# Kernel tuning notes

Hardware: AMD Instinct MI355X
Metric: run time of the kernel (lower is better)

The kernel has to match this reference:

```python
import jax, jax.numpy as jnp
import numpy as np
from jax import lax

K, N, DV, NBPS, NITER, BATCH = 1056, 2112, 5, 4, 20, 1024
M = N - K            # number of parity checks
E = M * (DV + 1)     # Tanner-graph edges (H = [A | I_m], row weight DV+1)
NSYM = N // NBPS     # QAM symbols per codeword


def _qam16():
    # Sionna-style Gray-mapped QAM constellation, unit average energy.
    def pam_gray(b):
        if len(b) > 1:
            return (1 - 2 * b[0]) * (2 ** (len(b) - 1) - pam_gray(b[1:]))
        return 1 - 2 * b[0]
    pts = []
    for i in range(2 ** NBPS):
        b = [(i >> (NBPS - 1 - j)) & 1 for j in range(NBPS)]
        pts.append(complex(pam_gray(b[0::2]), pam_gray(b[1::2])))
    pts = np.asarray(pts)
    pts = pts / np.sqrt(np.mean(np.abs(pts) ** 2))
    return pts.real.astype(np.float32), pts.imag.astype(np.float32)


def setup_inputs() -> dict:
    key = jax.random.key(0)
    rng = np.random.default_rng(0)
    bits = jnp.asarray(rng.integers(0, 2, size=(BATCH, K)), jnp.int32)
    # sparse A: DV distinct info-bit columns per check row
    a_idx = np.argsort(rng.random((M, K)), axis=1)[:, :DV].astype(np.int32)
    edge_vn = np.concatenate([a_idx, K + np.arange(M, dtype=np.int32)[:, None]], axis=1).reshape(-1)
    edge_cn = np.repeat(np.arange(M, dtype=np.int32), DV + 1)
    pre, pim = _qam16()
    k1, k2 = jax.random.split(key)
    return {
        "bits": bits,
        "a_idx": jnp.asarray(a_idx),
        "edge_cn": jnp.asarray(edge_cn),
        "edge_vn": jnp.asarray(edge_vn),
        "points_re": jnp.asarray(pre),
        "points_im": jnp.asarray(pim),
        "noise_re": jax.random.normal(k1, (BATCH, NSYM), jnp.float32),
        "noise_im": jax.random.normal(k2, (BATCH, NSYM), jnp.float32),
        "ebno_db": jnp.float32(4.0),
    }


def _forward(bits, a_idx, edge_cn, edge_vn, points_re, points_im, noise_re, noise_im, ebno_db):
    B = bits.shape[0]
    coderate = K / N
    # ebnodb2no (Es = 1): N0 = 1 / (EbN0_lin * coderate * bits_per_symbol)
    no = 1.0 / (10.0 ** (ebno_db / 10.0) * coderate * NBPS)
    # --- LDPC encode: H = [A | I], parity_i = XOR of info bits in row i ---
    parity = jnp.sum(bits[:, a_idx], axis=-1) % 2          # [B, M]
    cw = jnp.concatenate([bits, parity], axis=1)           # [B, N]
    # --- QAM map ---
    w = jnp.array([1 << (NBPS - 1 - j) for j in range(NBPS)], jnp.int32)
    sym = jnp.sum(cw.reshape(B, NSYM, NBPS) * w, axis=-1)  # [B, S]
    sigma = jnp.sqrt(no / 2.0)
    y_re = points_re[sym] + sigma * noise_re
    y_im = points_im[sym] + sigma * noise_im
    # --- APP demap: LLR = log p(b=0|y) - log p(b=1|y) ---
    d2 = (y_re[..., None] - points_re) ** 2 + (y_im[..., None] - points_im) ** 2  # [B,S,16]
    lg = (-d2 / no)[..., None]                                                     # [B,S,16,1]
    lab = (jnp.arange(2 ** NBPS)[:, None] >> jnp.arange(NBPS - 1, -1, -1)) & 1     # [16,4]
    NEG = jnp.float32(-1e30)
    l0 = jax.nn.logsumexp(jnp.where(lab == 0, lg, NEG), axis=2)
    l1 = jax.nn.logsumexp(jnp.where(lab == 1, lg, NEG), axis=2)
    llr = (l0 - l1).reshape(B, N)                          # [B, N]
    # --- sum-product BP, flooding schedule, NITER iterations ---
    def marg(c2v):  # scatter-add check->variable messages onto variable nodes
        return jnp.zeros((B, N), c2v.dtype).at[:, edge_vn].add(c2v)
    def step(c2v, _):
        v2c = (llr + marg(c2v))[:, edge_vn] - c2v          # extrinsic VN->CN [B,E]
        av = jnp.clip(jnp.abs(v2c), 1e-6, 20.0)
        lt = jnp.log(jnp.tanh(av * 0.5))                   # log|tanh(.)| <= 0
        sg = (v2c < 0).astype(v2c.dtype)
        cs = jnp.zeros((B, M), v2c.dtype).at[:, edge_cn].add(lt)
        ns = jnp.zeros((B, M), v2c.dtype).at[:, edge_cn].add(sg)
        ex = jnp.exp(jnp.minimum(cs[:, edge_cn] - lt, -1e-7))   # prod over other edges < 1
        sp = 1.0 - 2.0 * jnp.mod(ns[:, edge_cn] - sg, 2.0)      # sign product over other edges
        return sp * 2.0 * jnp.arctanh(ex), None
    c2v, _ = lax.scan(step, jnp.zeros((B, E), jnp.float32), None, length=NITER)
    tot = llr + marg(c2v)
    bits_rx = (tot[:, :K] < 0).astype(jnp.float32)         # hard_out=True
    return bits.astype(jnp.float32), bits_rx, tot[:, :K]


def reference(bits, a_idx, edge_cn, edge_vn, points_re, points_im, noise_re, noise_im, ebno_db):
    b, brx, _ = _forward(bits, a_idx, edge_cn, edge_vn, points_re, points_im,
                         noise_re, noise_im, ebno_db)
    return b, brx
```

## Files before the change

### kernel.cpp

```cpp
#include <hip/hip_runtime.h>

#define K_     1056
#define N_     2112
#define M_     1056
#define E_     6336
#define NIE_   5280
#define CAP_   6336
#define ALL_   7392
#define DV_    5
#define ROW_   6
#define NSYM_  528
#define NITER_ 20
#define BATCH_ 1024
#define BS_    512

#define LOG2E_ 1.4426950408889634f
#define AVLO_  (1e-6f * LOG2E_)
#define AVHI_  (20.0f * LOG2E_)
#define QC_    0.99999988f

__device__ __forceinline__ int seg_stride(int d) { return d | 1; }

__device__ __forceinline__ float fexp2(float x) { return __builtin_amdgcn_exp2f(x); }
__device__ __forceinline__ float flog2(float x) { return __builtin_amdgcn_logf(x); }
__device__ __forceinline__ float frcp(float x)  { return __builtin_amdgcn_rcpf(x); }

__global__ __launch_bounds__(BS_, 8) void link_kernel(
    const int*   __restrict__ bits,
    const int*   __restrict__ a_idx,
    const float* __restrict__ points_re,
    const float* __restrict__ points_im,
    const float* __restrict__ noise_re,
    const float* __restrict__ noise_im,
    const float* __restrict__ ebno_db,
    const int*   __restrict__ edge_vn,
    float*       __restrict__ out)
{
#pragma clang fp contract(off)
    const int b   = blockIdx.x;
    const int tid = threadIdx.x;

    __shared__ float s_all[ALL_];
    __shared__ float s_pre[16];
    __shared__ float s_pim[16];
    __shared__ int   s_hist[32];
    __shared__ int   s_binStart[32];
    __shared__ int   s_binBase[32];

    float* s_mem  = s_all;
    float* s_marg = s_all + CAP_;

    int* sc        = (int*)(s_all + N_);
    int* s_deg     = sc;
    int* s_perm    = sc + K_;
    int* s_offslot = sc + 2 * K_;
    int* s_cnt     = sc + 3 * K_;

    if (tid < 16) {
        s_pre[tid] = points_re[tid];
        s_pim[tid] = points_im[tid];
    }
    if (tid < 32) s_hist[tid] = 0;

    const float eb    = ebno_db[0];
    const float no    = 1.0f / ((powf(10.0f, eb / 10.0f) * 0.5f) * 4.0f);
    const float sigma = sqrtf(no / 2.0f);

    for (int i = tid; i < K_; i += BS_) {
        int v = bits[b * K_ + i];
        s_mem[i] = (float)v;
        out[b * K_ + i] = (float)v;
    }
    __syncthreads();

    for (int m = tid; m < M_; m += BS_) {
        float acc = 0.0f;
        #pragma unroll
        for (int d = 0; d < DV_; ++d) acc += s_mem[a_idx[m * DV_ + d]];
        s_mem[K_ + m] = (float)(((int)acc) & 1);
    }
    for (int v = tid; v < K_; v += BS_) { s_deg[v] = 0; s_cnt[v] = 0; }
    __syncthreads();

    for (int s = tid; s < NSYM_; s += BS_) {
        int c0 = (int)s_mem[4 * s + 0];
        int c1 = (int)s_mem[4 * s + 1];
        int c2 = (int)s_mem[4 * s + 2];
        int c3 = (int)s_mem[4 * s + 3];
        int sym = c0 * 8 + c1 * 4 + c2 * 2 + c3;
        float yre = s_pre[sym] + sigma * noise_re[b * NSYM_ + s];
        float yim = s_pim[sym] + sigma * noise_im[b * NSYM_ + s];
        #pragma unroll
        for (int j = 0; j < 4; ++j) {
            float m0 = -1e30f, m1 = -1e30f;
            #pragma unroll
            for (int p = 0; p < 16; ++p) {
                float dre  = yre - s_pre[p];
                float dim_ = yim - s_pim[p];
                float lg   = -(dre * dre + dim_ * dim_) / no;
                if (((p >> (3 - j)) & 1) == 0) m0 = fmaxf(m0, lg);
                else                           m1 = fmaxf(m1, lg);
            }
            float sum0 = 0.0f, sum1 = 0.0f;
            #pragma unroll
            for (int p = 0; p < 16; ++p) {
                float dre  = yre - s_pre[p];
                float dim_ = yim - s_pim[p];
                float lg   = -(dre * dre + dim_ * dim_) / no;
                if (((p >> (3 - j)) & 1) == 0) sum0 += __expf(lg - m0);
                else                           sum1 += __expf(lg - m1);
            }
            float llr = (m0 + __logf(sum0)) - (m1 + __logf(sum1));
            s_mem[4 * s + j] = llr * LOG2E_;
        }
    }
    for (int idx = tid; idx < NIE_; idx += BS_) {
        int m = idx / 5, j = idx - m * 5;
        atomicAdd(&s_deg[edge_vn[m * ROW_ + j]], 1);
    }
    __syncthreads();

    for (int v = tid; v < K_; v += BS_) atomicAdd(&s_hist[s_deg[v] & 31], 1);
    __syncthreads();
    if (tid == 0) {
        int accS = 0, accB = 0;
        for (int d = 0; d < 32; ++d) {
            int c = s_hist[d];
            s_binStart[d] = accS;
            s_binBase[d]  = accB;
            s_hist[d]     = accS;
            accS += c;
            accB += c * seg_stride(d);
        }
    }
    __syncthreads();
    for (int v = tid; v < K_; v += BS_) {
        int d    = s_deg[v];
        int slot = atomicAdd(&s_hist[d & 31], 1);
        int base = s_binBase[d] + (slot - s_binStart[d]) * seg_stride(d);
        s_perm[slot]  = v | (d << 16);
        s_offslot[v]  = base | (slot << 16);
    }
    __syncthreads();

    int      pv[3];
    unsigned od[3];
    float    lr[3];
    #pragma unroll
    for (int k = 0; k < 3; ++k) {
        int s = tid + BS_ * k;
        if (s < K_) {
            int w = s_perm[s];
            int v = w & 0xFFFF;
            int d = w >> 16;
            int base = s_binBase[d] + (s - s_binStart[d]) * seg_stride(d);
            pv[k] = v;
            od[k] = (unsigned)base | ((unsigned)d << 16);
            lr[k] = s_mem[v];
        } else { pv[k] = 0; od[k] = 0; lr[k] = 0.0f; }
    }
    float    t5[3];
    unsigned vnp[3][5];
    #pragma unroll
    for (int kk = 0; kk < 3; ++kk) {
        int m = tid + BS_ * kk;
        if (m < M_) {
            #pragma unroll
            for (int j = 0; j < 5; ++j) {
                int v = edge_vn[m * ROW_ + j];
                int r = atomicAdd(&s_cnt[v], 1);
                int w = s_offslot[v];
                vnp[kk][j]  = (unsigned)(w >> 16) | ((unsigned)((w & 0xFFFF) + r) << 16);
            }
            float lrP = s_mem[K_ + m];
            float av  = __builtin_amdgcn_fmed3f(fabsf(lrP), AVLO_, AVHI_);
            float e   = fexp2(-av);
            float tm  = (1.0f - e) * frcp(1.0f + e);
            t5[kk] = copysignf(tm, lrP);
        } else { t5[kk] = 0.0f; }
    }
    __syncthreads();
    for (int i = tid; i < CAP_; i += BS_) s_mem[i] = 0.0f;
    __syncthreads();

    for (int it = 0; it < NITER_; ++it) {
        #pragma unroll
        for (int k = 0; k < 3; ++k) {
            int s = tid + BS_ * k;
            if (s < K_) {
                int base = (int)(od[k] & 0xFFFFu);
                int dg   = (int)(od[k] >> 16);
                float mg = lr[k];
                int d = 0;
                for (; d + 1 < dg; d += 2) {
                    mg += s_mem[base + d];
                    mg += s_mem[base + d + 1];
                }
                if (d < dg) mg += s_mem[base + d];
                s_marg[s] = mg;
            }
        }
        __syncthreads();
        #pragma unroll
        for (int kk = 0; kk < 3; ++kk) {
            int m = tid + BS_ * kk;
            if (m < M_) {
                float tj[5];
                #pragma unroll
                for (int j = 0; j < 5; ++j) {
                    unsigned w = vnp[kk][j];
                    float v2c = s_marg[w & 0xFFFFu] - s_mem[w >> 16];
                    float av  = __builtin_amdgcn_fmed3f(fabsf(v2c), AVLO_, AVHI_);
                    float e   = fexp2(-av);
                    float tm  = (1.0f - e) * frcp(1.0f + e);
                    tj[j] = copysignf(tm, v2c);
                }
                float qv[5];
                float pr = t5[kk];
                #pragma unroll
                for (int j = 0; j < 5; ++j) { qv[j] = pr; pr *= tj[j]; }
                float sf = 1.0f;
                #pragma unroll
                for (int j = 4; j >= 0; --j) { qv[j] *= sf; sf *= tj[j]; }
                #pragma unroll
                for (int j = 0; j < 5; ++j) {
                    float q = __builtin_amdgcn_fmed3f(qv[j], -QC_, QC_);
                    float r = flog2((1.0f + q) * frcp(1.0f - q));
                    s_mem[vnp[kk][j] >> 16] = r;
                }
            }
        }
        __syncthreads();
    }

    #pragma unroll
    for (int k = 0; k < 3; ++k) {
        int s = tid + BS_ * k;
        if (s < K_) {
            int base = (int)(od[k] & 0xFFFFu);
            int dg   = (int)(od[k] >> 16);
            float mg = lr[k];
            int d = 0;
            for (; d + 1 < dg; d += 2) {
                mg += s_mem[base + d];
                mg += s_mem[base + d + 1];
            }
            if (d < dg) mg += s_mem[base + d];
            out[(size_t)BATCH_ * K_ + b * K_ + pv[k]] = (mg < 0.0f) ? 1.0f : 0.0f;
        }
    }
}

extern "C" void kernel_launch(void* const* d_in, const int* in_sizes, int n_in,
                              void* d_out, int out_size, void* d_ws, size_t ws_size,
                              hipStream_t stream) {
    const int*   bits    = (const int*)  d_in[0];
    const int*   a_idx   = (const int*)  d_in[1];
    const int*   edge_vn = (const int*)  d_in[3];
    const float* pre     = (const float*)d_in[4];
    const float* pim     = (const float*)d_in[5];
    const float* nre     = (const float*)d_in[6];
    const float* nim     = (const float*)d_in[7];
    const float* ebno    = (const float*)d_in[8];

    link_kernel<<<BATCH_, BS_, 0, stream>>>(bits, a_idx, pre, pim, nre, nim,
                                            ebno, edge_vn, (float*)d_out);
}
```

Before: 183.9 us.

## Write extrinsic VN messages in place and pack edge byte offsets

The variable-node pass now overwrites each edge slot in shared memory with the extrinsic message (marginal minus incoming) instead of storing a separate marginal array. The check-node pass then does a single LDS read per edge instead of two, and s_marg is dropped, which shrinks the shared-memory footprint. Edge addresses are stored as packed 16-bit byte offsets, two per register, cutting per-thread register use from 15 to 9. The cost is an extra read-modify-write loop per variable node in the VN phase. The smaller LDS and register footprint may also allow more blocks per CU.

```diff
diff --git a/kernel.cpp b/kernel.cpp
--- a/kernel.cpp
+++ b/kernel.cpp
@@ -6,7 +6,6 @@
 #define E_     6336
 #define NIE_   5280
 #define CAP_   6336
-#define ALL_   7392
 #define DV_    5
 #define ROW_   6
 #define NSYM_  528
@@ -40,15 +39,15 @@
     const int b   = blockIdx.x;
     const int tid = threadIdx.x;
 
-    __shared__ float s_all[ALL_];
+    __shared__ float s_all[CAP_];
     __shared__ float s_pre[16];
     __shared__ float s_pim[16];
     __shared__ int   s_hist[32];
     __shared__ int   s_binStart[32];
     __shared__ int   s_binBase[32];
 
-    float* s_mem  = s_all;
-    float* s_marg = s_all + CAP_;
+    float* s_mem = s_all;
+    char*  sb    = (char*)s_all;
 
     int* sc        = (int*)(s_all + N_);
     int* s_deg     = sc;
@@ -160,24 +159,32 @@
         } else { pv[k] = 0; od[k] = 0; lr[k] = 0.0f; }
     }
     float    t5[3];
-    unsigned vnp[3][5];
+    unsigned ep[3][3];
     #pragma unroll
     for (int kk = 0; kk < 3; ++kk) {
         int m = tid + BS_ * kk;
         if (m < M_) {
+            unsigned eb5[5];
             #pragma unroll
             for (int j = 0; j < 5; ++j) {
                 int v = edge_vn[m * ROW_ + j];
                 int r = atomicAdd(&s_cnt[v], 1);
                 int w = s_offslot[v];
-                vnp[kk][j]  = (unsigned)(w >> 16) | ((unsigned)((w & 0xFFFF) + r) << 16);
-            }
+                int epos = (w & 0xFFFF) + r;
+                eb5[j] = (unsigned)(epos << 2);
+            }
+            ep[kk][0] = eb5[0] | (eb5[1] << 16);
+            ep[kk][1] = eb5[2] | (eb5[3] << 16);
+            ep[kk][2] = eb5[4];
             float lrP = s_mem[K_ + m];
             float av  = __builtin_amdgcn_fmed3f(fabsf(lrP), AVLO_, AVHI_);
             float e   = fexp2(-av);
             float tm  = (1.0f - e) * frcp(1.0f + e);
             t5[kk] = copysignf(tm, lrP);
-        } else { t5[kk] = 0.0f; }
+        } else {
+            t5[kk] = 0.0f;
+            ep[kk][0] = 0; ep[kk][1] = 0; ep[kk][2] = 0;
+        }
     }
     __syncthreads();
     for (int i = tid; i < CAP_; i += BS_) s_mem[i] = 0.0f;
@@ -197,7 +204,8 @@
                     mg += s_mem[base + d + 1];
                 }
                 if (d < dg) mg += s_mem[base + d];
-                s_marg[s] = mg;
+                for (int i = 0; i < dg; ++i)
+                    s_mem[base + i] = mg - s_mem[base + i];
             }
         }
         __syncthreads();
@@ -205,11 +213,16 @@
         for (int kk = 0; kk < 3; ++kk) {
             int m = tid + BS_ * kk;
             if (m < M_) {
+                unsigned a0 =  ep[kk][0] & 0xFFFFu;
+                unsigned a1 =  ep[kk][0] >> 16;
+                unsigned a2 =  ep[kk][1] & 0xFFFFu;
+                unsigned a3 =  ep[kk][1] >> 16;
+                unsigned a4 =  ep[kk][2];
+                unsigned ad[5] = { a0, a1, a2, a3, a4 };
                 float tj[5];
                 #pragma unroll
                 for (int j = 0; j < 5; ++j) {
-                    unsigned w = vnp[kk][j];
-                    float v2c = s_marg[w & 0xFFFFu] - s_mem[w >> 16];
+                    float v2c = *(const float*)(sb + ad[j]);
                     float av  = __builtin_amdgcn_fmed3f(fabsf(v2c), AVLO_, AVHI_);
                     float e   = fexp2(-av);
                     float tm  = (1.0f - e) * frcp(1.0f + e);
@@ -226,7 +239,7 @@
                 for (int j = 0; j < 5; ++j) {
                     float q = __builtin_amdgcn_fmed3f(qv[j], -QC_, QC_);
                     float r = flog2((1.0f + q) * frcp(1.0f - q));
-                    s_mem[vnp[kk][j] >> 16] = r;
+                    *(float*)(sb + ad[j]) = r;
                 }
             }
         }
```

After: 192.5 us. 1.05x slower.
